# Performance work log

Measured on AMD Instinct MI355X. Metric: run time of the kernel, lower is better.

The kernel has to match this reference:

```python
import jax, jax.numpy as jnp
import numpy as np
from jax import lax

B, N, S, K, C = 8, 4096, 1024, 64, 64
RADIUS = 0.2
MLP = [64, 128, 256]
INT_MAX = jnp.iinfo(jnp.int32).max

_batched_gather = jax.vmap(lambda a, i: a[i])  # (N,D),(S,K)->(S,K,D)


def setup_inputs() -> dict:
    key = jax.random.key(0)
    ks = jax.random.split(key, 6)
    xyz = jax.random.uniform(ks[0], (B, N, 3), dtype=jnp.float32)
    points = jax.random.normal(ks[1], (B, N, C), dtype=jnp.float32)
    fps_inds = jax.random.randint(ks[2], (B, S), 0, N, dtype=jnp.int32)
    c_in = [3 + C] + MLP[:-1]
    w0 = jax.random.normal(ks[3], (c_in[0], MLP[0]), dtype=jnp.float32) * 0.1
    w1 = jax.random.normal(ks[4], (c_in[1], MLP[1]), dtype=jnp.float32) * 0.1
    w2 = jax.random.normal(ks[5], (c_in[2], MLP[2]), dtype=jnp.float32) * 0.1
    return {"xyz": xyz, "points": points, "fps_inds": fps_inds,
            "w0": w0, "w1": w1, "w2": w2}


def _query_ball_point(radius, nsample, xyz, new_xyz):
    # dists: (B, S, N)
    dists = jnp.linalg.norm(new_xyz[:, :, None, :] - xyz[:, None, :, :], axis=-1)
    # nsample nearest neighbors (ascending distance), like argsort[:, :, :nsample]
    neg_d, idx = lax.top_k(-dists, nsample)            # (B,S,K)
    valid = (-neg_d) < radius                          # prefix mask (dists ascending)
    idx_m = jnp.where(valid, idx, INT_MAX)
    sidx = jnp.sort(idx_m, axis=-1)
    # invalid slots -> first (smallest) valid index
    return jnp.where(valid, sidx, sidx[:, :, :1])


def reference(xyz, points, fps_inds, w0, w1, w2):
    new_xyz = _batched_gather(xyz, fps_inds)                       # (B,S,3)
    idx = _query_ball_point(RADIUS, K, xyz, new_xyz)               # (B,S,K)
    grouped_xyz = _batched_gather(xyz, idx) - new_xyz[:, :, None]  # (B,S,K,3)
    grouped_pts = _batched_gather(points, idx)                     # (B,S,K,C)
    feat = jnp.concatenate([grouped_xyz, grouped_pts], axis=-1)    # (B,S,K,3+C)
    for w in (w0, w1, w2):  # 1x1 conv == channel matmul, then relu
        feat = jax.nn.relu(jnp.einsum('bskc,cf->bskf', feat, w))
    new_points = jnp.max(feat, axis=2)                             # (B,S,F)
    return new_xyz, new_points
```

## Files before the change

kernel.cpp:

```cpp
#include <hip/hip_runtime.h>

#define NB 8
#define NN 4096
#define NS 1024
#define NC 64
#define OUT_PTS_OFF (NB*NS*3)
#define CAP 512
#define RB 0.2f
#define QPB 8

typedef __attribute__((ext_vector_type(8))) short bf16x8;
typedef __attribute__((ext_vector_type(4))) float f32x4;

static __device__ __forceinline__ short f2bf(float f){
  unsigned u = __float_as_uint(f);
  unsigned r = (u + 0x7FFFu + ((u>>16)&1u)) >> 16;
  return (short)r;
}
static __device__ __forceinline__ float bf2f(short s){
  return __uint_as_float(((unsigned)(unsigned short)s) << 16);
}

#define WS_PX1_SH   1048576
#define WS_WF_SH    3145728

__global__ __launch_bounds__(256) void prep_weights(
    const float* __restrict__ w0, const float* __restrict__ w1,
    const float* __restrict__ w2, short* __restrict__ ws)
{
  int e = blockIdx.x*256 + threadIdx.x;
  if (e >= 47104) return;
  float v = 0.f;
  if (e < 6144) {
    int j=e&7, l=(e>>3)&63, nt=(e>>9)&3, kt=e>>11;
    int k = kt*32 + ((l>>4)<<3) + j, n = nt*16 + (l&15);
    if (k < 64) v = w0[(3+k)*64 + n];
    else if (k < 67) v = w0[(k-64)*64 + n];
  } else if (e < 14336) {
    int e2=e-6144;
    int j=e2&7, l=(e2>>3)&63, nt=(e2>>9)&7, kt=e2>>12;
    int k = kt*32 + ((l>>4)<<3) + j, n = nt*16 + (l&15);
    v = w1[k*128 + n];
  } else {
    int e3=e-14336;
    int j=e3&7, l=(e3>>3)&63, nt=(e3>>9)&15, kt=e3>>13;
    int k = kt*32 + ((l>>4)<<3) + j, n = nt*16 + (l&15);
    v = w2[k*256 + n];
  }
  ws[e] = f2bf(v);
}

__global__ __launch_bounds__(256) void px1_kernel(
    const float* __restrict__ xyz, const float* __restrict__ points,
    const short* __restrict__ wsb, short* __restrict__ px1)
{
  const int tid = threadIdx.x;
  const int w = tid>>6, l = tid&63, lr = l&15, grp = l>>4;
  const int rowbase = blockIdx.x*64 + w*16;
  const int row = rowbase + lr;
  const float* prow = points + (size_t)row*NC;
  const float* xr   = xyz + (size_t)row*3;

  bf16x8 a0, a1, a2;
  {
    float4 u0 = *(const float4*)(prow + grp*8);
    float4 u1 = *(const float4*)(prow + grp*8 + 4);
    float4 u2 = *(const float4*)(prow + 32 + grp*8);
    float4 u3 = *(const float4*)(prow + 32 + grp*8 + 4);
    a0 = (bf16x8){f2bf(u0.x),f2bf(u0.y),f2bf(u0.z),f2bf(u0.w),f2bf(u1.x),f2bf(u1.y),f2bf(u1.z),f2bf(u1.w)};
    a1 = (bf16x8){f2bf(u2.x),f2bf(u2.y),f2bf(u2.z),f2bf(u2.w),f2bf(u3.x),f2bf(u3.y),f2bf(u3.z),f2bf(u3.w)};
    short e0=0,e1=0,e2v=0;
    if (grp==0) { e0=f2bf(xr[0]); e1=f2bf(xr[1]); e2v=f2bf(xr[2]); }
    a2 = (bf16x8){e0,e1,e2v,0,0,0,0,0};
  }
  f32x4 zero4 = {0.f,0.f,0.f,0.f};
  #pragma unroll
  for (int nt=0; nt<4; ++nt) {
    f32x4 acc = zero4;
    bf16x8 b0 = *(const bf16x8*)(wsb + (((0*4+nt)*64 + l)<<3));
    bf16x8 b1 = *(const bf16x8*)(wsb + (((1*4+nt)*64 + l)<<3));
    bf16x8 b2 = *(const bf16x8*)(wsb + (((2*4+nt)*64 + l)<<3));
    acc = __builtin_amdgcn_mfma_f32_16x16x32_bf16(a0, b0, acc, 0,0,0);
    acc = __builtin_amdgcn_mfma_f32_16x16x32_bf16(a1, b1, acc, 0,0,0);
    acc = __builtin_amdgcn_mfma_f32_16x16x32_bf16(a2, b2, acc, 0,0,0);
    #pragma unroll
    for (int i=0;i<4;++i)
      px1[(size_t)(rowbase + grp*4 + i)*64 + nt*16 + lr] = f2bf(acc[i]);
  }
}

__global__ __launch_bounds__(256) void select_kernel(
    const float* __restrict__ xyz, const int* __restrict__ fps_inds,
    int* __restrict__ gsidx, float* __restrict__ out)
{
  __shared__ unsigned int cand_d[CAP];
  __shared__ int cand_i[CAP];
  __shared__ int scnt[256];
  __shared__ int chunkbase[64];
  __shared__ int tmp64[64];
  __shared__ int sc0;

  const int q = blockIdx.x, b = q >> 10, tid = threadIdx.x;
  const float* xb = xyz + (size_t)b*NN*3;
  const int fps = fps_inds[q];
  const float qx = xb[fps*3+0], qy = xb[fps*3+1], qz = xb[fps*3+2];
  if (tid < 3) out[q*3+tid] = xb[fps*3+tid];

  unsigned int dbits[16]; unsigned int msk=0; int c=0;
  {
    const float4* xv = (const float4*)(xb + tid*48);
    #pragma unroll
    for (int g=0; g<4; ++g) {
      float4 v0 = xv[g*3], v1 = xv[g*3+1], v2 = xv[g*3+2];
      float px[4] = {v0.x, v0.w, v1.z, v2.y};
      float py[4] = {v0.y, v1.x, v1.w, v2.z};
      float pz[4] = {v0.z, v1.y, v2.x, v2.w};
      #pragma unroll
      for (int u=0; u<4; ++u) {
        float dx=__fsub_rn(qx,px[u]), dy=__fsub_rn(qy,py[u]), dz=__fsub_rn(qz,pz[u]);
        float d2=__fadd_rn(__fadd_rn(__fmul_rn(dx,dx),__fmul_rn(dy,dy)),__fmul_rn(dz,dz));
        float d = __fsqrt_rn(d2);
        dbits[g*4+u] = __float_as_uint(d);
        if (d < RB) { msk |= 1u<<(g*4+u); c++; }
      }
    }
  }
  scnt[tid] = c; __syncthreads();
  if (tid < 64) {
    int s = scnt[tid*4]+scnt[tid*4+1]+scnt[tid*4+2]+scnt[tid*4+3];
    int incl = s;
    #pragma unroll
    for (int off=1; off<64; off<<=1) {
      int vv = __shfl_up(incl, off, 64);
      if (tid >= off) incl += vv;
    }
    chunkbase[tid] = incl - s;
    if (tid == 63) sc0 = incl;
  }
  __syncthreads();
  int cnt = sc0; if (cnt > CAP) cnt = CAP;
  {
    int base = chunkbase[tid>>2];
    for (int u = (tid & ~3); u < tid; ++u) base += scnt[u];
    #pragma unroll
    for (int r=0; r<16; ++r) {
      if (msk & (1u<<r)) {
        if (base < CAP) { cand_d[base] = dbits[r]; cand_i[base] = tid*16+r; }
        base++;
      }
    }
  }
  __syncthreads();

  if (cnt > 64) {
    for (int j=tid; j<cnt; j+=256) {
      unsigned dj = cand_d[j]; int rk=0;
      for (int i=0;i<cnt;++i) { unsigned di=cand_d[i]; rk += (int)((di<dj) | ((di==dj) & (i<j))); }
      if (rk < 64) tmp64[rk] = cand_i[j];
    }
    __syncthreads();
    if (tid < 64) {
      int v = tmp64[tid]; int p=0;
      for (int u=0;u<64;++u) p += (tmp64[u] < v);
      gsidx[q*64 + p] = v;
    }
  } else {
    if (tid < 64) gsidx[q*64 + tid] = cand_i[tid < cnt ? tid : 0];
  }
}

__global__ __launch_bounds__(256,2) void mlp_kernel(
    const float* __restrict__ xyz, const int* __restrict__ fps_inds,
    const float* __restrict__ w0, const short* __restrict__ wsb,
    const short* __restrict__ px1, const int* __restrict__ gsidx,
    float* __restrict__ out)
{
  __shared__ short h2[2][64][136];
  __shared__ float q1s[QPB][64];
  __shared__ int sidx[QPB][64];

  const int tid = threadIdx.x;
  const int w = tid>>6, l = tid&63, lr = l&15, grp = l>>4;
  const int q0 = blockIdx.x*QPB;
  const int b = q0 >> 10;
  const float* xb = xyz + (size_t)b*NN*3;

  bf16x8 b3[4][4];
  #pragma unroll
  for (int kt=0; kt<4; ++kt)
    #pragma unroll
    for (int j=0; j<4; ++j)
      b3[kt][j] = *(const bf16x8*)(wsb + 14336 + (((kt*16 + w*4 + j)*64 + l)<<3));

  for (int e = tid; e < QPB*64; e += 256) {
    int qq = e>>6, t = e&63;
    int fp = fps_inds[q0+qq];
    sidx[qq][t] = gsidx[(q0+qq)*64 + t];
    q1s[qq][t] = xb[fp*3]*w0[t] + xb[fp*3+1]*w0[64+t] + xb[fp*3+2]*w0[128+t];
  }
  if (tid < QPB*3) {
    int qq = tid/3, c = tid - qq*3;
    int fp = fps_inds[q0+qq];
    out[(q0+qq)*3 + c] = xb[fp*3+c];
  }
  __syncthreads();

  const short* px1b = px1 + (size_t)b*NN*64;
  const int myrow = w*16 + lr;

  bf16x8 v0, v1;
  {
    int idx = sidx[0][myrow];
    v0 = *(const bf16x8*)(px1b + idx*64 + grp*8);
    v1 = *(const bf16x8*)(px1b + idx*64 + 32 + grp*8);
  }

  f32x4 zero4 = {0.f,0.f,0.f,0.f};

  for (int qq = 0; qq < QPB; ++qq) {
    const int p = qq & 1;

    bf16x8 a20, a21;
    #pragma unroll
    for (int j=0;j<8;++j) {
      a20[j] = f2bf(fmaxf(bf2f(v0[j]) - q1s[qq][grp*8+j], 0.f));
      a21[j] = f2bf(fmaxf(bf2f(v1[j]) - q1s[qq][32+grp*8+j], 0.f));
    }
    if (qq+1 < QPB) {
      int idx = sidx[qq+1][myrow];
      v0 = *(const bf16x8*)(px1b + idx*64 + grp*8);
      v1 = *(const bf16x8*)(px1b + idx*64 + 32 + grp*8);
    }

    #pragma unroll
    for (int nt=0; nt<8; ++nt) {
      f32x4 acc = zero4;
      bf16x8 w10 = *(const bf16x8*)(wsb + 6144 + (((0*8+nt)*64 + l)<<3));
      bf16x8 w11 = *(const bf16x8*)(wsb + 6144 + (((1*8+nt)*64 + l)<<3));
      acc = __builtin_amdgcn_mfma_f32_16x16x32_bf16(a20, w10, acc, 0,0,0);
      acc = __builtin_amdgcn_mfma_f32_16x16x32_bf16(a21, w11, acc, 0,0,0);
      #pragma unroll
      for (int i=0;i<4;++i)
        h2[p][w*16 + grp*4 + i][nt*16 + lr] = f2bf(fmaxf(acc[i], 0.f));
    }
    __syncthreads();

    f32x4 acc3[4][4];
    #pragma unroll
    for (int mt=0; mt<4; ++mt)
      #pragma unroll
      for (int j=0; j<4; ++j) acc3[mt][j] = zero4;
    #pragma unroll
    for (int kt=0; kt<4; ++kt)
      #pragma unroll
      for (int mt=0; mt<4; ++mt) {
        bf16x8 a = *(const bf16x8*)&h2[p][mt*16 + lr][kt*32 + grp*8];
        #pragma unroll
        for (int j=0; j<4; ++j)
          acc3[mt][j] = __builtin_amdgcn_mfma_f32_16x16x32_bf16(a, b3[kt][j], acc3[mt][j], 0,0,0);
      }
    #pragma unroll
    for (int j=0; j<4; ++j) {
      float m = 0.f;
      #pragma unroll
      for (int mt=0; mt<4; ++mt)
        #pragma unroll
        for (int i=0; i<4; ++i) m = fmaxf(m, acc3[mt][j][i]);
      m = fmaxf(m, __shfl_xor(m, 16, 64));
      m = fmaxf(m, __shfl_xor(m, 32, 64));
      if (grp == 0) out[OUT_PTS_OFF + (q0+qq)*256 + (w*4+j)*16 + lr] = m;
    }
  }
}

extern "C" void kernel_launch(void* const* d_in, const int* in_sizes, int n_in,
                              void* d_out, int out_size, void* d_ws, size_t ws_size,
                              hipStream_t stream) {
  const float* xyz      = (const float*)d_in[0];
  const float* points   = (const float*)d_in[1];
  const int*   fps_inds = (const int*)d_in[2];
  const float* w0       = (const float*)d_in[3];
  const float* w1       = (const float*)d_in[4];
  const float* w2       = (const float*)d_in[5];
  float* out = (float*)d_out;

  int*   gsidx = (int*)d_ws;
  short* px1   = (short*)d_ws + WS_PX1_SH;
  short* wsb   = (short*)d_ws + WS_WF_SH;

  hipLaunchKernelGGL(prep_weights, dim3(184), dim3(256), 0, stream, w0, w1, w2, wsb);
  hipLaunchKernelGGL(px1_kernel,   dim3(512), dim3(256), 0, stream, xyz, points, wsb, px1);
  hipLaunchKernelGGL(select_kernel,dim3(NB*NS), dim3(256), 0, stream, xyz, fps_inds, gsidx, out);
  hipLaunchKernelGGL(mlp_kernel,   dim3(NB*NS/QPB), dim3(256), 0, stream,
                     xyz, fps_inds, w0, wsb, px1, gsidx, out);
}
```

Measured before the change: 110.8 us.

## Batch two queries per select block, stage W1 in LDS, swizzle h2 layout

The select kernel now handles two queries per block and loads the point coordinates into registers once for both, halving the grid. The MLP kernel stages W1 in shared memory instead of reading it from global memory on every query. It also uses a single XOR-swizzled h2 buffer with packed bf16 conversion via v_cvt_pk_bf16_f32, and raises the occupancy hint to 4 blocks. The W2 packing is permuted to match the swizzled column order. The costs are an extra barrier per query and tighter register limits under the higher occupancy bound.

```diff
diff --git a/kernel.cpp b/kernel.cpp
--- a/kernel.cpp
+++ b/kernel.cpp
@@ -19,6 +19,11 @@
 }
 static __device__ __forceinline__ float bf2f(short s){
   return __uint_as_float(((unsigned)(unsigned short)s) << 16);
+}
+static __device__ __forceinline__ unsigned cvtpk(float a, float b){
+  unsigned r;
+  asm("v_cvt_pk_bf16_f32 %0, %1, %2" : "=v"(r) : "v"(a), "v"(b));
+  return r;
 }
 
 #define WS_PX1_SH   1048576
@@ -44,7 +49,9 @@
   } else {
     int e3=e-14336;
     int j=e3&7, l=(e3>>3)&63, nt=(e3>>9)&15, kt=e3>>13;
-    int k = kt*32 + ((l>>4)<<3) + j, n = nt*16 + (l&15);
+    int p = kt*32 + ((l>>4)<<3) + j;
+    int k = ((p&7)<<4) + (p>>3);
+    int n = nt*16 + (l&15);
     v = w2[k*256 + n];
   }
   ws[e] = f2bf(v);
@@ -100,82 +107,91 @@
   __shared__ int tmp64[64];
   __shared__ int sc0;
 
-  const int q = blockIdx.x, b = q >> 10, tid = threadIdx.x;
+  const int q0 = blockIdx.x*2;
+  const int b = q0 >> 10, tid = threadIdx.x;
   const float* xb = xyz + (size_t)b*NN*3;
-  const int fps = fps_inds[q];
-  const float qx = xb[fps*3+0], qy = xb[fps*3+1], qz = xb[fps*3+2];
-  if (tid < 3) out[q*3+tid] = xb[fps*3+tid];
-
-  unsigned int dbits[16]; unsigned int msk=0; int c=0;
+
+  float px[16], py[16], pz[16];
   {
     const float4* xv = (const float4*)(xb + tid*48);
     #pragma unroll
     for (int g=0; g<4; ++g) {
       float4 v0 = xv[g*3], v1 = xv[g*3+1], v2 = xv[g*3+2];
-      float px[4] = {v0.x, v0.w, v1.z, v2.y};
-      float py[4] = {v0.y, v1.x, v1.w, v2.z};
-      float pz[4] = {v0.z, v1.y, v2.x, v2.w};
-      #pragma unroll
-      for (int u=0; u<4; ++u) {
-        float dx=__fsub_rn(qx,px[u]), dy=__fsub_rn(qy,py[u]), dz=__fsub_rn(qz,pz[u]);
-        float d2=__fadd_rn(__fadd_rn(__fmul_rn(dx,dx),__fmul_rn(dy,dy)),__fmul_rn(dz,dz));
-        float d = __fsqrt_rn(d2);
-        dbits[g*4+u] = __float_as_uint(d);
-        if (d < RB) { msk |= 1u<<(g*4+u); c++; }
-      }
-    }
-  }
-  scnt[tid] = c; __syncthreads();
-  if (tid < 64) {
-    int s = scnt[tid*4]+scnt[tid*4+1]+scnt[tid*4+2]+scnt[tid*4+3];
-    int incl = s;
-    #pragma unroll
-    for (int off=1; off<64; off<<=1) {
-      int vv = __shfl_up(incl, off, 64);
-      if (tid >= off) incl += vv;
-    }
-    chunkbase[tid] = incl - s;
-    if (tid == 63) sc0 = incl;
-  }
-  __syncthreads();
-  int cnt = sc0; if (cnt > CAP) cnt = CAP;
-  {
-    int base = chunkbase[tid>>2];
-    for (int u = (tid & ~3); u < tid; ++u) base += scnt[u];
+      px[g*4+0]=v0.x; px[g*4+1]=v0.w; px[g*4+2]=v1.z; px[g*4+3]=v2.y;
+      py[g*4+0]=v0.y; py[g*4+1]=v1.x; py[g*4+2]=v1.w; py[g*4+3]=v2.z;
+      pz[g*4+0]=v0.z; pz[g*4+1]=v1.y; pz[g*4+2]=v2.x; pz[g*4+3]=v2.w;
+    }
+  }
+
+  for (int qq = 0; qq < 2; ++qq) {
+    if (qq) __syncthreads();
+    const int q = q0 + qq;
+    const int fps = fps_inds[q];
+    const float qx = xb[fps*3+0], qy = xb[fps*3+1], qz = xb[fps*3+2];
+    if (tid < 3) out[q*3+tid] = xb[fps*3+tid];
+
+    unsigned int dbits[16]; unsigned int msk=0; int c=0;
     #pragma unroll
     for (int r=0; r<16; ++r) {
-      if (msk & (1u<<r)) {
-        if (base < CAP) { cand_d[base] = dbits[r]; cand_i[base] = tid*16+r; }
-        base++;
-      }
-    }
-  }
-  __syncthreads();
-
-  if (cnt > 64) {
-    for (int j=tid; j<cnt; j+=256) {
-      unsigned dj = cand_d[j]; int rk=0;
-      for (int i=0;i<cnt;++i) { unsigned di=cand_d[i]; rk += (int)((di<dj) | ((di==dj) & (i<j))); }
-      if (rk < 64) tmp64[rk] = cand_i[j];
+      float dx=__fsub_rn(qx,px[r]), dy=__fsub_rn(qy,py[r]), dz=__fsub_rn(qz,pz[r]);
+      float d2=__fadd_rn(__fadd_rn(__fmul_rn(dx,dx),__fmul_rn(dy,dy)),__fmul_rn(dz,dz));
+      float d = __fsqrt_rn(d2);
+      dbits[r] = __float_as_uint(d);
+      if (d < RB) { msk |= 1u<<r; c++; }
+    }
+    scnt[tid] = c; __syncthreads();
+    if (tid < 64) {
+      int s = scnt[tid*4]+scnt[tid*4+1]+scnt[tid*4+2]+scnt[tid*4+3];
+      int incl = s;
+      #pragma unroll
+      for (int off=1; off<64; off<<=1) {
+        int vv = __shfl_up(incl, off, 64);
+        if (tid >= off) incl += vv;
+      }
+      chunkbase[tid] = incl - s;
+      if (tid == 63) sc0 = incl;
     }
     __syncthreads();
-    if (tid < 64) {
-      int v = tmp64[tid]; int p=0;
-      for (int u=0;u<64;++u) p += (tmp64[u] < v);
-      gsidx[q*64 + p] = v;
-    }
-  } else {
-    if (tid < 64) gsidx[q*64 + tid] = cand_i[tid < cnt ? tid : 0];
-  }
-}
-
-__global__ __launch_bounds__(256,2) void mlp_kernel(
+    int cnt = sc0; if (cnt > CAP) cnt = CAP;
+    {
+      int base = chunkbase[tid>>2];
+      for (int u = (tid & ~3); u < tid; ++u) base += scnt[u];
+      #pragma unroll
+      for (int r=0; r<16; ++r) {
+        if (msk & (1u<<r)) {
+          if (base < CAP) { cand_d[base] = dbits[r]; cand_i[base] = tid*16+r; }
+          base++;
+        }
+      }
+    }
+    __syncthreads();
+
+    if (cnt > 64) {
+      for (int j=tid; j<cnt; j+=256) {
+        unsigned dj = cand_d[j]; int rk=0;
+        for (int i=0;i<cnt;++i) { unsigned di=cand_d[i]; rk += (int)((di<dj) | ((di==dj) & (i<j))); }
+        if (rk < 64) tmp64[rk] = cand_i[j];
+      }
+      __syncthreads();
+      if (tid < 64) {
+        int v = tmp64[tid]; int p=0;
+        for (int u=0;u<64;++u) p += (tmp64[u] < v);
+        gsidx[q*64 + p] = v;
+      }
+    } else {
+      if (tid < 64) gsidx[q*64 + tid] = cand_i[tid < cnt ? tid : 0];
+    }
+  }
+}
+
+__global__ __launch_bounds__(256,4) void mlp_kernel(
     const float* __restrict__ xyz, const int* __restrict__ fps_inds,
     const float* __restrict__ w0, const short* __restrict__ wsb,
     const short* __restrict__ px1, const int* __restrict__ gsidx,
     float* __restrict__ out)
 {
-  __shared__ short h2[2][64][136];
+  __shared__ __align__(16) short w1s[16*64*8];
+  __shared__ __align__(16) short h2[64][136];
   __shared__ float q1s[QPB][64];
   __shared__ int sidx[QPB][64];
 
@@ -192,6 +208,11 @@
     for (int j=0; j<4; ++j)
       b3[kt][j] = *(const bf16x8*)(wsb + 14336 + (((kt*16 + w*4 + j)*64 + l)<<3));
 
+  #pragma unroll
+  for (int e = 0; e < 4; ++e) {
+    int s = tid + e*256;
+    *(bf16x8*)&w1s[s*8] = *(const bf16x8*)(wsb + 6144 + s*8);
+  }
   for (int e = tid; e < QPB*64; e += 256) {
     int qq = e>>6, t = e&63;
     int fp = fps_inds[q0+qq];
@@ -218,13 +239,21 @@
   f32x4 zero4 = {0.f,0.f,0.f,0.f};
 
   for (int qq = 0; qq < QPB; ++qq) {
-    const int p = qq & 1;
+    if (qq) __syncthreads();
 
     bf16x8 a20, a21;
-    #pragma unroll
-    for (int j=0;j<8;++j) {
-      a20[j] = f2bf(fmaxf(bf2f(v0[j]) - q1s[qq][grp*8+j], 0.f));
-      a21[j] = f2bf(fmaxf(bf2f(v1[j]) - q1s[qq][32+grp*8+j], 0.f));
+    {
+      union { unsigned u[4]; bf16x8 v; } ua, ub;
+      #pragma unroll
+      for (int jp=0; jp<4; ++jp) {
+        float x0 = fmaxf(bf2f(v0[2*jp  ]) - q1s[qq][grp*8+2*jp  ], 0.f);
+        float x1 = fmaxf(bf2f(v0[2*jp+1]) - q1s[qq][grp*8+2*jp+1], 0.f);
+        ua.u[jp] = cvtpk(x0, x1);
+        float y0 = fmaxf(bf2f(v1[2*jp  ]) - q1s[qq][32+grp*8+2*jp  ], 0.f);
+        float y1 = fmaxf(bf2f(v1[2*jp+1]) - q1s[qq][32+grp*8+2*jp+1], 0.f);
+        ub.u[jp] = cvtpk(y0, y1);
+      }
+      a20 = ua.v; a21 = ub.v;
     }
     if (qq+1 < QPB) {
       int idx = sidx[qq+1][myrow];
@@ -233,15 +262,23 @@
     }
 
     #pragma unroll
-    for (int nt=0; nt<8; ++nt) {
-      f32x4 acc = zero4;
-      bf16x8 w10 = *(const bf16x8*)(wsb + 6144 + (((0*8+nt)*64 + l)<<3));
-      bf16x8 w11 = *(const bf16x8*)(wsb + 6144 + (((1*8+nt)*64 + l)<<3));
-      acc = __builtin_amdgcn_mfma_f32_16x16x32_bf16(a20, w10, acc, 0,0,0);
-      acc = __builtin_amdgcn_mfma_f32_16x16x32_bf16(a21, w11, acc, 0,0,0);
-      #pragma unroll
-      for (int i=0;i<4;++i)
-        h2[p][w*16 + grp*4 + i][nt*16 + lr] = f2bf(fmaxf(acc[i], 0.f));
+    for (int ntp=0; ntp<4; ++ntp) {
+      f32x4 accA = zero4, accB = zero4;
+      bf16x8 bA0 = *(const bf16x8*)&w1s[((0*8 + 2*ntp  )*64 + l)*8];
+      bf16x8 bA1 = *(const bf16x8*)&w1s[((1*8 + 2*ntp  )*64 + l)*8];
+      bf16x8 bB0 = *(const bf16x8*)&w1s[((0*8 + 2*ntp+1)*64 + l)*8];
+      bf16x8 bB1 = *(const bf16x8*)&w1s[((1*8 + 2*ntp+1)*64 + l)*8];
+      accA = __builtin_amdgcn_mfma_f32_16x16x32_bf16(a20, bA0, accA, 0,0,0);
+      accA = __builtin_amdgcn_mfma_f32_16x16x32_bf16(a21, bA1, accA, 0,0,0);
+      accB = __builtin_amdgcn_mfma_f32_16x16x32_bf16(a20, bB0, accB, 0,0,0);
+      accB = __builtin_amdgcn_mfma_f32_16x16x32_bf16(a21, bB1, accB, 0,0,0);
+      #pragma unroll
+      for (int i=0; i<4; ++i) {
+        int row = w*16 + grp*4 + i;
+        unsigned u = cvtpk(fmaxf(accA[i],0.f), fmaxf(accB[i],0.f));
+        int colb = (lr*16 + ntp*4) ^ ((row&7)<<4);
+        *(unsigned*)((char*)&h2[row][0] + colb) = u;
+      }
     }
     __syncthreads();
 
@@ -254,7 +291,9 @@
     for (int kt=0; kt<4; ++kt)
       #pragma unroll
       for (int mt=0; mt<4; ++mt) {
-        bf16x8 a = *(const bf16x8*)&h2[p][mt*16 + lr][kt*32 + grp*8];
+        int row = mt*16 + lr;
+        int colb = (kt*64 + grp*16) ^ ((row&7)<<4);
+        bf16x8 a = *(const bf16x8*)((const char*)&h2[row][0] + colb);
         #pragma unroll
         for (int j=0; j<4; ++j)
           acc3[mt][j] = __builtin_amdgcn_mfma_f32_16x16x32_bf16(a, b3[kt][j], acc3[mt][j], 0,0,0);
@@ -263,9 +302,10 @@
     for (int j=0; j<4; ++j) {
       float m = 0.f;
       #pragma unroll
-      for (int mt=0; mt<4; ++mt)
-        #pragma unroll
-        for (int i=0; i<4; ++i) m = fmaxf(m, acc3[mt][j][i]);
+      for (int mt=0; mt<4; ++mt) {
+        f32x4 t = acc3[mt][j];
+        m = fmaxf(m, fmaxf(fmaxf(t[0],t[1]), fmaxf(t[2],t[3])));
+      }
       m = fmaxf(m, __shfl_xor(m, 16, 64));
       m = fmaxf(m, __shfl_xor(m, 32, 64));
       if (grp == 0) out[OUT_PTS_OFF + (q0+qq)*256 + (w*4+j)*16 + lr] = m;
@@ -290,7 +330,7 @@
 
   hipLaunchKernelGGL(prep_weights, dim3(184), dim3(256), 0, stream, w0, w1, w2, wsb);
   hipLaunchKernelGGL(px1_kernel,   dim3(512), dim3(256), 0, stream, xyz, points, wsb, px1);
-  hipLaunchKernelGGL(select_kernel,dim3(NB*NS), dim3(256), 0, stream, xyz, fps_inds, gsidx, out);
+  hipLaunchKernelGGL(select_kernel,dim3(NB*NS/2), dim3(256), 0, stream, xyz, fps_inds, gsidx, out);
   hipLaunchKernelGGL(mlp_kernel,   dim3(NB*NS/QPB), dim3(256), 0, stream,
                      xyz, fps_inds, w0, wsb, px1, gsidx, out);
 }
```

Result: slower. 196.5 us (+77.3%).
